# Kernel tuning notes

Hardware: AMD Instinct MI355X
Metric: run time of the kernel (lower is better)

The kernel has to match this reference:

```python
import jax, jax.numpy as jnp
import numpy as np

B, T, C = 2, 2048, 2048
H, HKV, D = 16, 4, 128
R = 64  # rope_dim = head_dim * rotary_pct


def setup_inputs() -> dict:
    key = jax.random.key(0)
    ks = jax.random.split(key, 8)
    s = 0.02
    return {
        "x": jax.random.normal(ks[0], (B, T, C), jnp.float32),
        "cos": jnp.cos(jax.random.normal(ks[1], (T, R), jnp.float32)),
        "sin": jnp.sin(jax.random.normal(ks[2], (T, R), jnp.float32)),
        "Wq": jax.random.normal(ks[3], (C, C), jnp.float32) * s,
        "Wk": jax.random.normal(ks[4], (C, HKV * D), jnp.float32) * s,
        "Wv": jax.random.normal(ks[5], (C, HKV * D), jnp.float32) * s,
        "Wo": jax.random.normal(ks[6], (C, C), jnp.float32) * s,
        "gate": jax.random.normal(ks[7], (H,), jnp.float32) * 0.1 - 3.0,
    }


def _rotate_half(t):
    t1, t2 = t[..., : t.shape[-1] // 2], t[..., t.shape[-1] // 2:]
    return jnp.concatenate([-t2, t1], axis=-1)


def reference(x, cos, sin, Wq, Wk, Wv, Wo, gate):
    # projections -> (B, heads, T, D)
    q = (x @ Wq).reshape(B, T, H, D).transpose(0, 2, 1, 3)
    k = (x @ Wk).reshape(B, T, HKV, D).transpose(0, 2, 1, 3)
    v = (x @ Wv).reshape(B, T, HKV, D).transpose(0, 2, 1, 3)

    # partial RoPE on first R dims; cos/sin (T,R) broadcast over (B,h,T,R)
    q_r = q[..., :R] * cos + _rotate_half(q[..., :R]) * sin
    k_r = k[..., :R] * cos + _rotate_half(k[..., :R]) * sin
    q = jnp.concatenate([q_r, q[..., R:]], axis=-1)
    k = jnp.concatenate([k_r, k[..., R:]], axis=-1)

    # GQA: repeat_interleave kv heads to match H
    rep = H // HKV
    k = jnp.repeat(k, rep, axis=1)
    v = jnp.repeat(v, rep, axis=1)

    scale = D ** -0.5
    att = jnp.einsum("bhtd,bhsd->bhts", q, k) * scale  # (B,H,T,T)
    causal = jnp.tril(jnp.ones((T, T), bool))
    att = jnp.where(causal, att, -jnp.inf)
    att = jax.nn.softmax(att, axis=-1)

    # post-softmax learned per-head threshold gate
    thr = jax.nn.sigmoid(gate)[None, :, None, None]
    att = att * (att >= thr).astype(att.dtype)

    y = jnp.einsum("bhts,bhsd->bhtd", att, v)
    y = y.transpose(0, 2, 1, 3).reshape(B, T, C)
    return y @ Wo
```

## Files before the change

### kernel.cpp

```cpp
#include <hip/hip_runtime.h>
#include <stdint.h>

#define Bdim 2
#define Tdim 2048
#define Cdim 2048
#define Hdim 16
#define HKVdim 4
#define KVdim 512
#define KT 32

typedef __attribute__((ext_vector_type(8))) short bf16x8;
typedef __attribute__((ext_vector_type(4))) float f32x4;

#define GLOAD16(gp, lp) __builtin_amdgcn_global_load_lds( \
    (const __attribute__((address_space(1))) void*)(gp),  \
    (__attribute__((address_space(3))) void*)(lp), 16, 0, 0)
#define WAITV(N) asm volatile("s_waitcnt vmcnt(" #N ")" ::: "memory")
#define WAITL0() asm volatile("s_waitcnt lgkmcnt(0)" ::: "memory")

__device__ __forceinline__ unsigned short f2bf(float f) {
  union { float f; unsigned u; } a; a.f = f;
  unsigned u = a.u + 0x7FFFu + ((a.u >> 16) & 1u);
  return (unsigned short)(u >> 16);
}
__device__ __forceinline__ float bf2f(unsigned short h) {
  union { float f; unsigned u; } a; a.u = ((unsigned)h) << 16;
  return a.f;
}

__global__ void split_x_kernel(const float* __restrict__ x, unsigned short* __restrict__ hi,
                               unsigned short* __restrict__ lo, int n) {
  int i = blockIdx.x * blockDim.x + threadIdx.x;
  int stride = gridDim.x * blockDim.x;
  for (; i < n; i += stride) {
    float f = x[i];
    unsigned short hb = f2bf(f);
    hi[i] = hb;
    lo[i] = f2bf(f - bf2f(hb));
  }
}

__global__ void transpose_split_kernel(const float* __restrict__ in, unsigned short* __restrict__ hi,
                                       unsigned short* __restrict__ lo, int K, int N) {
  __shared__ float tile[32][33];
  int k0 = blockIdx.x * 32, n0 = blockIdx.y * 32;
  int tx = threadIdx.x, ty = threadIdx.y;
#pragma unroll
  for (int i = 0; i < 32; i += 8)
    tile[ty + i][tx] = in[(size_t)(k0 + ty + i) * N + n0 + tx];
  __syncthreads();
#pragma unroll
  for (int i = 0; i < 32; i += 8) {
    float f = tile[tx][ty + i];
    size_t o = (size_t)(n0 + ty + i) * K + k0 + tx;
    unsigned short hb = f2bf(f);
    hi[o] = hb;
    if (lo) lo[o] = f2bf(f - bf2f(hb));
  }
}

__global__ __launch_bounds__(512, 4) void qkv8_kernel(
    const unsigned short* __restrict__ xhi, const unsigned short* __restrict__ xlo,
    const unsigned short* __restrict__ WqThi, const unsigned short* __restrict__ WqTlo,
    const unsigned short* __restrict__ WkThi, const unsigned short* __restrict__ WkTlo,
    const unsigned short* __restrict__ WvThi,
    const float* __restrict__ cs, const float* __restrict__ sn,
    unsigned short* __restrict__ qhi, unsigned short* __restrict__ qlo,
    unsigned short* __restrict__ khi, unsigned short* __restrict__ klo,
    unsigned short* __restrict__ vun)
{
  __shared__ char sL[3][24576];
  int tid = threadIdx.x, wid = tid >> 6, lane = tid & 63;
  int bid = blockIdx.x;
  int mode, bm, bn;
  if (bid < 256)      { mode = 0; bm = bid >> 3; bn = bid & 7; }
  else if (bid < 320) { int i = bid - 256; mode = 1; bm = i >> 1; bn = i & 1; }
  else                { int i = bid - 320; mode = 2; bm = i >> 1; bn = i & 1; }
  const unsigned short *Bhp, *Blp = WqTlo;
  if (mode == 0)      { Bhp = WqThi; Blp = WqTlo; }
  else if (mode == 1) { Bhp = WkThi; Blp = WkTlo; }
  else                { Bhp = WvThi; }
  int nk = (mode == 2) ? 64 : 192;

  const char* xh = (const char*)xhi;
  const char* xl = (const char*)xlo;
  const char* Bh = (const char*)Bhp;
  const char* Bl = (const char*)Blp;
  size_t arow0 = (size_t)bm * 128;
  size_t brow0 = (size_t)bn * 256;

  int wrow = (wid >> 2) & 1, wcol = wid & 3;
  int ln15 = lane & 15, j16 = (lane >> 4) * 16;

  f32x4 acc[4][4];
#pragma unroll
  for (int rf = 0; rf < 4; ++rf)
#pragma unroll
    for (int cf = 0; cf < 4; ++cf)
      acc[rf][cf] = f32x4{0.f, 0.f, 0.f, 0.f};

  auto stage = [&](int buf, int kt) {
    int reg = kt >> 6;
    int kk2 = (kt & 63) * 64;
    const char* As = (reg == 1) ? xl : xh;
    const char* Bs = (reg == 2) ? Bl : Bh;
    {
      int o = tid * 16; int row = o >> 6; int c = (o & 63) ^ ((row & 3) << 4);
      GLOAD16(As + (arow0 + row) * 4096 + kk2 + c, &sL[buf][o]);
    }
#pragma unroll
    for (int i = 0; i < 2; ++i) {
      int o = (i * 512 + tid) * 16; int row = o >> 6; int c = (o & 63) ^ ((row & 3) << 4);
      GLOAD16(Bs + (brow0 + row) * 4096 + kk2 + c, &sL[buf][8192 + o]);
    }
  };

  stage(0, 0); stage(1, 1); stage(2, 2);
  WAITV(6);
  __builtin_amdgcn_s_barrier();

  int cb = 0;
  for (int kt = 0; kt < nk; ++kt) {
    bf16x8 a[4], b[4];
    const char* base = sL[cb];
#pragma unroll
    for (int rf = 0; rf < 4; ++rf) {
      int r = wrow * 64 + rf * 16 + ln15;
      a[rf] = *(const bf16x8*)(base + r * 64 + (j16 ^ ((r & 3) << 4)));
    }
#pragma unroll
    for (int cf = 0; cf < 4; ++cf) {
      int r = wcol * 64 + cf * 16 + ln15;
      b[cf] = *(const bf16x8*)(base + 8192 + r * 64 + (j16 ^ ((r & 3) << 4)));
    }
    WAITL0();
    __builtin_amdgcn_sched_barrier(0);
    __builtin_amdgcn_s_barrier();
    if (kt + 3 < nk)      { stage(cb, kt + 3); WAITV(6); }
    else if (kt + 2 < nk) { WAITV(3); }
    else                  { WAITV(0); }
    __builtin_amdgcn_s_setprio(1);
#pragma unroll
    for (int rf = 0; rf < 4; ++rf)
#pragma unroll
      for (int cf = 0; cf < 4; ++cf)
        acc[rf][cf] = __builtin_amdgcn_mfma_f32_16x16x32_bf16(a[rf], b[cf], acc[rf][cf], 0, 0, 0);
    __builtin_amdgcn_s_setprio(0);
    __builtin_amdgcn_s_barrier();
    cb = (cb == 2) ? 0 : cb + 1;
  }

  if (mode <= 1) {
    int nh = (mode == 0) ? Hdim : HKVdim;
    unsigned short* oph = (mode == 0) ? qhi : khi;
    unsigned short* opl = (mode == 0) ? qlo : klo;
#pragma unroll
    for (int rf = 0; rf < 4; ++rf)
#pragma unroll
      for (int rr = 0; rr < 4; ++rr) {
        int rowl = wrow * 64 + rf * 16 + (lane >> 4) * 4 + rr;
        int grow = bm * 128 + rowl;
        int t = grow & (Tdim - 1), bb = grow >> 11;
#pragma unroll
        for (int cf = 0; cf < 4; ++cf) {
          int ncol = wcol * 64 + cf * 16 + ln15;
          int h = bn * 2 + (ncol >> 7);
          int d = ncol & 127;
          float o;
          if ((wcol & 1) == 0) {
            float c = cs[t * 64 + d], s = sn[t * 64 + d];
            o = (cf < 2) ? (acc[rf][cf][rr] * c - acc[rf][cf + 2][rr] * s)
                         : (acc[rf][cf][rr] * c + acc[rf][cf - 2][rr] * s);
          } else o = acc[rf][cf][rr];
          size_t ob = (((size_t)(bb * nh + h)) * Tdim + t) * 128 + d;
          unsigned short hb = f2bf(o);
          oph[ob] = hb;
          opl[ob] = f2bf(o - bf2f(hb));
        }
      }
  } else {
#pragma unroll
    for (int rf = 0; rf < 4; ++rf)
#pragma unroll
      for (int rr = 0; rr < 4; ++rr) {
        int rowl = wrow * 64 + rf * 16 + (lane >> 4) * 4 + rr;
        int grow = bm * 128 + rowl;
        int t = grow & (Tdim - 1), bb = grow >> 11;
#pragma unroll
        for (int cf = 0; cf < 4; ++cf) {
          int ncol = wcol * 64 + cf * 16 + ln15;
          int g = bn * 2 + (ncol >> 7);
          int d = ncol & 127;
          vun[(((size_t)(bb * HKVdim + g)) * Tdim + t) * 128 + d] = f2bf(acc[rf][cf][rr]);
        }
      }
  }
}

__global__ __launch_bounds__(512, 4) void wo8_kernel(
    const unsigned short* __restrict__ A, const unsigned short* __restrict__ Bt,
    float* __restrict__ C)
{
  __shared__ char sL[3][24576];
  int tid = threadIdx.x, wid = tid >> 6, lane = tid & 63;
  int bm = blockIdx.x >> 3, bn = blockIdx.x & 7;
  const char* As = (const char*)A;
  const char* Bs = (const char*)Bt;
  size_t arow0 = (size_t)bm * 128;
  size_t brow0 = (size_t)bn * 256;
  int wrow = (wid >> 2) & 1, wcol = wid & 3;
  int ln15 = lane & 15, j16 = (lane >> 4) * 16;
  const int nk = 64;

  f32x4 acc[4][4];
#pragma unroll
  for (int rf = 0; rf < 4; ++rf)
#pragma unroll
    for (int cf = 0; cf < 4; ++cf)
      acc[rf][cf] = f32x4{0.f, 0.f, 0.f, 0.f};

  auto stage = [&](int buf, int kt) {
    int kk2 = kt * 64;
    {
      int o = tid * 16; int row = o >> 6; int c = (o & 63) ^ ((row & 3) << 4);
      GLOAD16(As + (arow0 + row) * 4096 + kk2 + c, &sL[buf][o]);
    }
#pragma unroll
    for (int i = 0; i < 2; ++i) {
      int o = (i * 512 + tid) * 16; int row = o >> 6; int c = (o & 63) ^ ((row & 3) << 4);
      GLOAD16(Bs + (brow0 + row) * 4096 + kk2 + c, &sL[buf][8192 + o]);
    }
  };

  stage(0, 0); stage(1, 1); stage(2, 2);
  WAITV(6);
  __builtin_amdgcn_s_barrier();

  int cb = 0;
  for (int kt = 0; kt < nk; ++kt) {
    bf16x8 a[4], b[4];
    const char* base = sL[cb];
#pragma unroll
    for (int rf = 0; rf < 4; ++rf) {
      int r = wrow * 64 + rf * 16 + ln15;
      a[rf] = *(const bf16x8*)(base + r * 64 + (j16 ^ ((r & 3) << 4)));
    }
#pragma unroll
    for (int cf = 0; cf < 4; ++cf) {
      int r = wcol * 64 + cf * 16 + ln15;
      b[cf] = *(const bf16x8*)(base + 8192 + r * 64 + (j16 ^ ((r & 3) << 4)));
    }
    WAITL0();
    __builtin_amdgcn_sched_barrier(0);
    __builtin_amdgcn_s_barrier();
    if (kt + 3 < nk)      { stage(cb, kt + 3); WAITV(6); }
    else if (kt + 2 < nk) { WAITV(3); }
    else                  { WAITV(0); }
    __builtin_amdgcn_s_setprio(1);
#pragma unroll
    for (int rf = 0; rf < 4; ++rf)
#pragma unroll
      for (int cf = 0; cf < 4; ++cf)
        acc[rf][cf] = __builtin_amdgcn_mfma_f32_16x16x32_bf16(a[rf], b[cf], acc[rf][cf], 0, 0, 0);
    __builtin_amdgcn_s_setprio(0);
    __builtin_amdgcn_s_barrier();
    cb = (cb == 2) ? 0 : cb + 1;
  }

#pragma unroll
  for (int rf = 0; rf < 4; ++rf)
#pragma unroll
    for (int rr = 0; rr < 4; ++rr) {
      int grow = bm * 128 + wrow * 64 + rf * 16 + (lane >> 4) * 4 + rr;
#pragma unroll
      for (int cf = 0; cf < 4; ++cf) {
        int gcol = bn * 256 + wcol * 64 + cf * 16 + ln15;
        C[(size_t)grow * Cdim + gcol] = acc[rf][cf][rr];
      }
    }
}

__global__ void transpose_v_bf16_kernel(const unsigned short* __restrict__ vsrc,
                                        unsigned short* __restrict__ vt) {
  __shared__ unsigned short tile[32][33];
  int bg = blockIdx.x;
  int t0 = blockIdx.y * 32, d0 = blockIdx.z * 32;
  int tx = threadIdx.x, ty = threadIdx.y;
#pragma unroll
  for (int i = 0; i < 32; i += 8)
    tile[ty + i][tx] = vsrc[((size_t)bg * Tdim + t0 + ty + i) * 128 + d0 + tx];
  __syncthreads();
#pragma unroll
  for (int i = 0; i < 32; i += 8)
    vt[((size_t)(bg * 128 + d0 + ty + i)) * Tdim + t0 + tx] = tile[tx][ty + i];
}

__global__ __launch_bounds__(512, 4) void attn_kernel(
    const unsigned short* __restrict__ qhi, const unsigned short* __restrict__ qlo,
    const unsigned short* __restrict__ khi, const unsigned short* __restrict__ klo,
    const unsigned short* __restrict__ vt, const float* __restrict__ gate,
    unsigned short* __restrict__ y)
{
  __shared__ alignas(16) unsigned short sKh[2][KT * 128];
  __shared__ alignas(16) unsigned short sKl[2][KT * 128];
  __shared__ alignas(16) unsigned short sV[2][128 * KT];
  __shared__ alignas(16) unsigned short sP[8][16 * 40];
  __shared__ float sBM[8][64];

  int qb = (gridDim.x - 1) - blockIdx.x;
  int bh = blockIdx.y;
  int b = bh >> 4, h = bh & 15;
  int g = h >> 2;
  int t0 = qb * 128;
  int tid = threadIdx.x, wid = tid >> 6, lane = tid & 63;
  int ln15 = lane & 15, j16 = (lane >> 4) * 16, ro4 = (lane >> 4) * 4;
  const float cs2 = 0.08838834764831845f * 1.4426950408889634f;
  const float M2  = 8.0f * 1.4426950408889634f;

  const unsigned short* kh_base = khi + (((size_t)b * HKVdim + g) * Tdim) * 128;
  const unsigned short* kl_base = klo + (((size_t)b * HKVdim + g) * Tdim) * 128;
  const unsigned short* v_base  = vt  + (((size_t)b * HKVdim + g) * 128) * (size_t)Tdim;

  bf16x8 aqh[4], aql[4];
  {
    size_t qoff = ((((size_t)b * Hdim + h) * Tdim) + t0 + wid * 16 + ln15) * 128 + (lane >> 4) * 8;
#pragma unroll
    for (int kf = 0; kf < 4; ++kf) {
      aqh[kf] = *(const bf16x8*)(qhi + qoff + kf * 32);
      aql[kf] = *(const bf16x8*)(qlo + qoff + kf * 32);
    }
  }
  float thr = 1.f / (1.f + expf(-gate[h]));

  int nkb = (qb + 1) * 4;
  int tq_lo = t0 + wid * 16;

  auto stageK = [&](int buf, int kb) {
    int o = wid * 1024 + lane * 16;
    int row = o >> 8;
    int col = (o & 255) ^ ((row & 7) << 4);
    size_t goff = ((size_t)(kb * KT + row)) * 256 + col;
    GLOAD16((const char*)kh_base + goff, (char*)sKh[buf] + wid * 1024);
    GLOAD16((const char*)kl_base + goff, (char*)sKl[buf] + wid * 1024);
  };
  auto stageV = [&](int buf, int kb) {
    int o = wid * 1024 + lane * 16;
    int row = o >> 6;
    int col = (o & 63) ^ (((row ^ (row >> 2)) & 3) << 4);
    size_t goff = (size_t)row * (Tdim * 2) + (size_t)kb * 64 + col;
    GLOAD16((const char*)v_base + goff, (char*)sV[buf] + wid * 1024);
  };
  auto qk = [&](int buf, f32x4* s) {
    __builtin_amdgcn_s_setprio(1);
#pragma unroll
    for (int nf = 0; nf < 2; ++nf) {
      f32x4 a = {0.f, 0.f, 0.f, 0.f};
      int krow = nf * 16 + ln15;
      int sw = (krow & 7) << 4;
#pragma unroll
      for (int kf = 0; kf < 4; ++kf) {
        int boff = (kf * 64 + j16) ^ sw;
        bf16x8 bh_ = *(const bf16x8*)((const char*)sKh[buf] + krow * 256 + boff);
        bf16x8 bl_ = *(const bf16x8*)((const char*)sKl[buf] + krow * 256 + boff);
        a = __builtin_amdgcn_mfma_f32_16x16x32_bf16(aqh[kf], bh_, a, 0, 0, 0);
        a = __builtin_amdgcn_mfma_f32_16x16x32_bf16(aql[kf], bh_, a, 0, 0, 0);
        a = __builtin_amdgcn_mfma_f32_16x16x32_bf16(aqh[kf], bl_, a, 0, 0, 0);
      }
      s[nf] = a;
    }
    __builtin_amdgcn_s_setprio(0);
  };

  float lloc[4];
#pragma unroll
  for (int r = 0; r < 4; ++r) lloc[r] = 0.f;

  stageK(0, 0);
  __syncthreads();
  for (int kb = 0; kb < nkb; ++kb) {
    int buf = kb & 1;
    if (kb + 1 < nkb) stageK(buf ^ 1, kb + 1);
    if (kb * KT <= tq_lo + 15) {
      f32x4 s[2];
      qk(buf, s);
      float wmax = -1e30f;
      bool full = (kb * KT + KT - 1) <= tq_lo;
      if (full) {
#pragma unroll
        for (int nf = 0; nf < 2; ++nf)
#pragma unroll
          for (int r = 0; r < 4; ++r) {
            float v = s[nf][r] * cs2;
            wmax = fmaxf(wmax, v);
            lloc[r] += __builtin_exp2f(v - M2);
          }
      } else {
#pragma unroll
        for (int nf = 0; nf < 2; ++nf) {
          int tk = kb * KT + nf * 16 + ln15;
#pragma unroll
          for (int r = 0; r < 4; ++r) {
            int tq = tq_lo + ro4 + r;
            float v = (tk <= tq) ? s[nf][r] * cs2 : -1e30f;
            wmax = fmaxf(wmax, v);
            lloc[r] += __builtin_exp2f(v - M2);
          }
        }
      }
#pragma unroll
      for (int off = 1; off < 64; off <<= 1)
        wmax = fmaxf(wmax, __shfl_xor(wmax, off));
      if (lane == 0) sBM[wid][kb] = wmax;
    }
    __syncthreads();
  }

  float lrow[4], lgate2[4];
#pragma unroll
  for (int r = 0; r < 4; ++r) {
    float l = lloc[r];
#pragma unroll
    for (int off = 1; off < 16; off <<= 1) l += __shfl_xor(l, off);
    lrow[r] = l;
    lgate2[r] = __log2f(thr * l) + M2;
  }
  float lgmin = fminf(fminf(lgate2[0], lgate2[1]), fminf(lgate2[2], lgate2[3]));
  lgmin = fminf(lgmin, __shfl_xor(lgmin, 16));
  lgmin = fminf(lgmin, __shfl_xor(lgmin, 32));

  f32x4 yacc[8];
#pragma unroll
  for (int n = 0; n < 8; ++n) yacc[n] = f32x4{0.f, 0.f, 0.f, 0.f};

  stageK(0, 0);
  stageV(0, 0);
  __syncthreads();
  for (int kb = 0; kb < nkb; ++kb) {
    int buf = kb & 1;
    if (kb + 1 < nkb) { stageK(buf ^ 1, kb + 1); stageV(buf ^ 1, kb + 1); }
    if (kb * KT <= tq_lo + 15 && sBM[wid][kb] >= lgmin) {
      f32x4 s[2];
      qk(buf, s);
      bool anyk = false;
      float pv[2][4];
      bool full = (kb * KT + KT - 1) <= tq_lo;
#pragma unroll
      for (int nf = 0; nf < 2; ++nf) {
        int tk = kb * KT + nf * 16 + ln15;
#pragma unroll
        for (int r = 0; r < 4; ++r) {
          int tq = tq_lo + ro4 + r;
          float v = s[nf][r] * cs2;
          bool keep = (full || tk <= tq) && (v >= lgate2[r]);
          float p = 0.f;
          if (keep) { p = __builtin_exp2f(v - M2); anyk = true; }
          pv[nf][r] = p;
        }
      }
      if (__any(anyk)) {
#pragma unroll
        for (int nf = 0; nf < 2; ++nf)
#pragma unroll
          for (int r = 0; r < 4; ++r)
            sP[wid][(ro4 + r) * 40 + nf * 16 + ln15] = f2bf(pv[nf][r]);
        __builtin_amdgcn_s_setprio(1);
        bf16x8 pa = *(const bf16x8*)&sP[wid][ln15 * 40 + (lane >> 4) * 8];
#pragma unroll
        for (int nf2 = 0; nf2 < 8; ++nf2) {
          int vrow = nf2 * 16 + ln15;
          int vboff = j16 ^ (((vrow ^ (vrow >> 2)) & 3) << 4);
          bf16x8 vb = *(const bf16x8*)((const char*)sV[buf] + vrow * 64 + vboff);
          yacc[nf2] = __builtin_amdgcn_mfma_f32_16x16x32_bf16(pa, vb, yacc[nf2], 0, 0, 0);
        }
        __builtin_amdgcn_s_setprio(0);
      }
    }
    __syncthreads();
  }

#pragma unroll
  for (int r = 0; r < 4; ++r) {
    int tq = t0 + wid * 16 + ro4 + r;
    float invl = 1.f / lrow[r];
    size_t base = ((size_t)(b * Tdim + tq)) * Cdim + h * 128;
#pragma unroll
    for (int nf2 = 0; nf2 < 8; ++nf2)
      y[base + nf2 * 16 + ln15] = f2bf(yacc[nf2][r] * invl);
  }
}

extern "C" void kernel_launch(void* const* d_in, const int* in_sizes, int n_in,
                              void* d_out, int out_size, void* d_ws, size_t ws_size,
                              hipStream_t stream)
{
  (void)in_sizes; (void)n_in; (void)out_size; (void)ws_size;
  const float* x    = (const float*)d_in[0];
  const float* cosT = (const float*)d_in[1];
  const float* sinT = (const float*)d_in[2];
  const float* Wq   = (const float*)d_in[3];
  const float* Wk   = (const float*)d_in[4];
  const float* Wv   = (const float*)d_in[5];
  const float* Wo   = (const float*)d_in[6];
  const float* gate = (const float*)d_in[7];
  float* out = (float*)d_out;

  char* ws = (char*)d_ws;
  size_t off = 0;
  auto alloc = [&](size_t bytes) -> char* {
    char* p = ws + off; off += (bytes + 255) & ~(size_t)255; return p;
  };
  const size_t NX = (size_t)Bdim * Tdim * Cdim;
  const size_t NK = (size_t)Bdim * Tdim * KVdim;

  unsigned short* xhi   = (unsigned short*)alloc(NX * 2);
  unsigned short* xlo   = (unsigned short*)alloc(NX * 2);
  unsigned short* WqThi = (unsigned short*)alloc((size_t)Cdim * Cdim * 2);
  unsigned short* WqTlo = (unsigned short*)alloc((size_t)Cdim * Cdim * 2);
  unsigned short* WkThi = (unsigned short*)alloc((size_t)Cdim * KVdim * 2);
  unsigned short* WkTlo = (unsigned short*)alloc((size_t)Cdim * KVdim * 2);
  unsigned short* WvThi = (unsigned short*)alloc((size_t)Cdim * KVdim * 2);
  unsigned short* WoThi = (unsigned short*)alloc((size_t)Cdim * Cdim * 2);
  unsigned short* qhi   = (unsigned short*)alloc(NX * 2);
  unsigned short* qlo   = (unsigned short*)alloc(NX * 2);
  unsigned short* khi   = (unsigned short*)alloc(NK * 2);
  unsigned short* klo   = (unsigned short*)alloc(NK * 2);
  unsigned short* vun   = (unsigned short*)alloc(NK * 2);
  unsigned short* vtr   = (unsigned short*)alloc(NK * 2);
  unsigned short* yb    = (unsigned short*)alloc(NX * 2);

  dim3 tb(32, 8);
  split_x_kernel<<<2048, 256, 0, stream>>>(x, xhi, xlo, (int)NX);
  transpose_split_kernel<<<dim3(64, 64), tb, 0, stream>>>(Wq, WqThi, WqTlo, Cdim, Cdim);
  transpose_split_kernel<<<dim3(64, 16), tb, 0, stream>>>(Wk, WkThi, WkTlo, Cdim, KVdim);
  transpose_split_kernel<<<dim3(64, 16), tb, 0, stream>>>(Wv, WvThi, nullptr, Cdim, KVdim);
  transpose_split_kernel<<<dim3(64, 64), tb, 0, stream>>>(Wo, WoThi, nullptr, Cdim, Cdim);

  qkv8_kernel<<<384, 512, 0, stream>>>(
      xhi, xlo, WqThi, WqTlo, WkThi, WkTlo, WvThi,
      cosT, sinT, qhi, qlo, khi, klo, vun);
  transpose_v_bf16_kernel<<<dim3(8, 64, 4), tb, 0, stream>>>(vun, vtr);

  attn_kernel<<<dim3(16, 32), 512, 0, stream>>>(qhi, qlo, khi, klo, vtr, gate, yb);

  wo8_kernel<<<256, 512, 0, stream>>>(yb, WoThi, out);
}
```

Baseline: 427.4 us.

## Enlarge GEMM tiles to 256x256 with 4-stage split A/B ping-pong pipeline

Both the QKV and Wo GEMM kernels move from 128x256 to 256x256 output tiles per block, with each wave computing 128x64. Staging goes from a 3-buffer to a 4-buffer ring, and the A and B global-to-LDS loads are split so they interleave with two half-MFMA phases. The LDS swizzle pattern also changes. The aim is more operand reuse per LDS load and better overlap of loads with compute, at the cost of halving the grid (192 and 128 blocks on a 256-CU part), which leaves CUs idle and raises register and LDS pressure.

```diff
diff --git a/kernel.cpp b/kernel.cpp
--- a/kernel.cpp
+++ b/kernel.cpp
@@ -17,6 +17,7 @@
     (__attribute__((address_space(3))) void*)(lp), 16, 0, 0)
 #define WAITV(N) asm volatile("s_waitcnt vmcnt(" #N ")" ::: "memory")
 #define WAITL0() asm volatile("s_waitcnt lgkmcnt(0)" ::: "memory")
+#define SWZ(r) ((((r) >> 1) & 3) << 4)
 
 __device__ __forceinline__ unsigned short f2bf(float f) {
   union { float f; unsigned u; } a; a.f = f;
@@ -59,7 +60,8 @@
   }
 }
 
-__global__ __launch_bounds__(512, 4) void qkv8_kernel(
+
+__global__ __launch_bounds__(512, 2) void qkv8p_kernel(
     const unsigned short* __restrict__ xhi, const unsigned short* __restrict__ xlo,
     const unsigned short* __restrict__ WqThi, const unsigned short* __restrict__ WqTlo,
     const unsigned short* __restrict__ WkThi, const unsigned short* __restrict__ WkTlo,
@@ -69,13 +71,13 @@
     unsigned short* __restrict__ khi, unsigned short* __restrict__ klo,
     unsigned short* __restrict__ vun)
 {
-  __shared__ char sL[3][24576];
+  __shared__ char sL[4][32768];
   int tid = threadIdx.x, wid = tid >> 6, lane = tid & 63;
   int bid = blockIdx.x;
   int mode, bm, bn;
-  if (bid < 256)      { mode = 0; bm = bid >> 3; bn = bid & 7; }
-  else if (bid < 320) { int i = bid - 256; mode = 1; bm = i >> 1; bn = i & 1; }
-  else                { int i = bid - 320; mode = 2; bm = i >> 1; bn = i & 1; }
+  if (bid < 128)      { mode = 0; bm = bid >> 3; bn = bid & 7; }
+  else if (bid < 160) { int i = bid - 128; mode = 1; bm = i >> 1; bn = i & 1; }
+  else                { int i = bid - 160; mode = 2; bm = i >> 1; bn = i & 1; }
   const unsigned short *Bhp, *Blp = WqTlo;
   if (mode == 0)      { Bhp = WqThi; Blp = WqTlo; }
   else if (mode == 1) { Bhp = WkThi; Blp = WkTlo; }
@@ -86,68 +88,99 @@
   const char* xl = (const char*)xlo;
   const char* Bh = (const char*)Bhp;
   const char* Bl = (const char*)Blp;
-  size_t arow0 = (size_t)bm * 128;
+  size_t arow0 = (size_t)bm * 256;
   size_t brow0 = (size_t)bn * 256;
 
-  int wrow = (wid >> 2) & 1, wcol = wid & 3;
-  int ln15 = lane & 15, j16 = (lane >> 4) * 16;
-
-  f32x4 acc[4][4];
-#pragma unroll
-  for (int rf = 0; rf < 4; ++rf)
+  int wrow = wid >> 2, wcol = wid & 3;
+  int ln15 = lane & 15, cbk = (lane >> 4) * 16;
+
+  f32x4 acc[8][4];
+#pragma unroll
+  for (int rf = 0; rf < 8; ++rf)
 #pragma unroll
     for (int cf = 0; cf < 4; ++cf)
       acc[rf][cf] = f32x4{0.f, 0.f, 0.f, 0.f};
 
-  auto stage = [&](int buf, int kt) {
+  auto stageA = [&](int buf, int kt) {
     int reg = kt >> 6;
-    int kk2 = (kt & 63) * 64;
     const char* As = (reg == 1) ? xl : xh;
+    size_t kb = (size_t)(kt & 63) * 64;
+#pragma unroll
+    for (int i = 0; i < 2; ++i) {
+      int o = i * 8192 + tid * 16;
+      int row = o >> 6;
+      int c = (o & 63) ^ SWZ(row);
+      GLOAD16(As + (arow0 + row) * 4096 + kb + c, &sL[buf][o]);
+    }
+  };
+  auto stageB = [&](int buf, int kt) {
+    int reg = kt >> 6;
     const char* Bs = (reg == 2) ? Bl : Bh;
-    {
-      int o = tid * 16; int row = o >> 6; int c = (o & 63) ^ ((row & 3) << 4);
-      GLOAD16(As + (arow0 + row) * 4096 + kk2 + c, &sL[buf][o]);
-    }
+    size_t kb = (size_t)(kt & 63) * 64;
 #pragma unroll
     for (int i = 0; i < 2; ++i) {
-      int o = (i * 512 + tid) * 16; int row = o >> 6; int c = (o & 63) ^ ((row & 3) << 4);
-      GLOAD16(Bs + (brow0 + row) * 4096 + kk2 + c, &sL[buf][8192 + o]);
-    }
-  };
-
-  stage(0, 0); stage(1, 1); stage(2, 2);
-  WAITV(6);
+      int o = i * 8192 + tid * 16;
+      int row = o >> 6;
+      int c = (o & 63) ^ SWZ(row);
+      GLOAD16(Bs + (brow0 + row) * 4096 + kb + c, &sL[buf][16384 + o]);
+    }
+  };
+
+  stageA(0, 0); stageB(0, 0);
+  stageA(1, 1); stageB(1, 1);
+  stageA(2, 2); stageB(2, 2);
+  WAITV(8);
   __builtin_amdgcn_s_barrier();
 
-  int cb = 0;
-  for (int kt = 0; kt < nk; ++kt) {
-    bf16x8 a[4], b[4];
-    const char* base = sL[cb];
+  for (int j = 0; j < nk; ++j) {
+    const char* base = sL[j & 3];
+    int sb = (j + 3) & 3;
+    bf16x8 a0[4], a1[4], b[4];
 #pragma unroll
     for (int rf = 0; rf < 4; ++rf) {
-      int r = wrow * 64 + rf * 16 + ln15;
-      a[rf] = *(const bf16x8*)(base + r * 64 + (j16 ^ ((r & 3) << 4)));
+      int r = wrow * 128 + rf * 16 + ln15;
+      a0[rf] = *(const bf16x8*)(base + r * 64 + (cbk ^ SWZ(r)));
     }
 #pragma unroll
     for (int cf = 0; cf < 4; ++cf) {
       int r = wcol * 64 + cf * 16 + ln15;
-      b[cf] = *(const bf16x8*)(base + 8192 + r * 64 + (j16 ^ ((r & 3) << 4)));
-    }
+      b[cf] = *(const bf16x8*)(base + 16384 + r * 64 + (cbk ^ SWZ(r)));
+    }
+    if (j + 3 < nk) stageA(sb, j + 3);
+    __builtin_amdgcn_s_barrier();
     WAITL0();
     __builtin_amdgcn_sched_barrier(0);
-    __builtin_amdgcn_s_barrier();
-    if (kt + 3 < nk)      { stage(cb, kt + 3); WAITV(6); }
-    else if (kt + 2 < nk) { WAITV(3); }
-    else                  { WAITV(0); }
     __builtin_amdgcn_s_setprio(1);
 #pragma unroll
     for (int rf = 0; rf < 4; ++rf)
 #pragma unroll
       for (int cf = 0; cf < 4; ++cf)
-        acc[rf][cf] = __builtin_amdgcn_mfma_f32_16x16x32_bf16(a[rf], b[cf], acc[rf][cf], 0, 0, 0);
+        acc[rf][cf] = __builtin_amdgcn_mfma_f32_16x16x32_bf16(a0[rf], b[cf], acc[rf][cf], 0, 0, 0);
     __builtin_amdgcn_s_setprio(0);
     __builtin_amdgcn_s_barrier();
-    cb = (cb == 2) ? 0 : cb + 1;
+#pragma unroll
+    for (int rf = 0; rf < 4; ++rf) {
+      int r = wrow * 128 + 64 + rf * 16 + ln15;
+      a1[rf] = *(const bf16x8*)(base + r * 64 + (cbk ^ SWZ(r)));
+    }
+    if (j + 3 < nk) stageB(sb, j + 3);
+    __builtin_amdgcn_s_barrier();
+    WAITL0();
+    __builtin_amdgcn_sched_barrier(0);
+    __builtin_amdgcn_s_setprio(1);
+#pragma unroll
+    for (int rf = 0; rf < 4; ++rf)
+#pragma unroll
+      for (int cf = 0; cf < 4; ++cf)
+        acc[rf + 4][cf] = __builtin_amdgcn_mfma_f32_16x16x32_bf16(a1[rf], b[cf], acc[rf + 4][cf], 0, 0, 0);
+    __builtin_amdgcn_s_setprio(0);
+    {
+      int rem = nk - j - 2;
+      if (rem >= 2)      { WAITV(8); }
+      else if (rem == 1) { WAITV(4); }
+      else if (rem == 0) { WAITV(0); }
+    }
+    __builtin_amdgcn_s_barrier();
   }
 
   if (mode <= 1) {
@@ -155,11 +188,10 @@
     unsigned short* oph = (mode == 0) ? qhi : khi;
     unsigned short* opl = (mode == 0) ? qlo : klo;
 #pragma unroll
-    for (int rf = 0; rf < 4; ++rf)
+    for (int rf = 0; rf < 8; ++rf)
 #pragma unroll
       for (int rr = 0; rr < 4; ++rr) {
-        int rowl = wrow * 64 + rf * 16 + (lane >> 4) * 4 + rr;
-        int grow = bm * 128 + rowl;
+        int grow = bm * 256 + wrow * 128 + rf * 16 + (lane >> 4) * 4 + rr;
         int t = grow & (Tdim - 1), bb = grow >> 11;
 #pragma unroll
         for (int cf = 0; cf < 4; ++cf) {
@@ -180,11 +212,10 @@
       }
   } else {
 #pragma unroll
-    for (int rf = 0; rf < 4; ++rf)
+    for (int rf = 0; rf < 8; ++rf)
 #pragma unroll
       for (int rr = 0; rr < 4; ++rr) {
-        int rowl = wrow * 64 + rf * 16 + (lane >> 4) * 4 + rr;
-        int grow = bm * 128 + rowl;
+        int grow = bm * 256 + wrow * 128 + rf * 16 + (lane >> 4) * 4 + rr;
         int t = grow & (Tdim - 1), bb = grow >> 11;
 #pragma unroll
         for (int cf = 0; cf < 4; ++cf) {
@@ -197,81 +228,111 @@
   }
 }
 
-__global__ __launch_bounds__(512, 4) void wo8_kernel(
+__global__ __launch_bounds__(512, 2) void wo8p_kernel(
     const unsigned short* __restrict__ A, const unsigned short* __restrict__ Bt,
     float* __restrict__ C)
 {
-  __shared__ char sL[3][24576];
+  __shared__ char sL[4][32768];
   int tid = threadIdx.x, wid = tid >> 6, lane = tid & 63;
   int bm = blockIdx.x >> 3, bn = blockIdx.x & 7;
   const char* As = (const char*)A;
   const char* Bs = (const char*)Bt;
-  size_t arow0 = (size_t)bm * 128;
+  size_t arow0 = (size_t)bm * 256;
   size_t brow0 = (size_t)bn * 256;
-  int wrow = (wid >> 2) & 1, wcol = wid & 3;
-  int ln15 = lane & 15, j16 = (lane >> 4) * 16;
+  int wrow = wid >> 2, wcol = wid & 3;
+  int ln15 = lane & 15, cbk = (lane >> 4) * 16;
   const int nk = 64;
 
-  f32x4 acc[4][4];
-#pragma unroll
-  for (int rf = 0; rf < 4; ++rf)
+  f32x4 acc[8][4];
+#pragma unroll
+  for (int rf = 0; rf < 8; ++rf)
 #pragma unroll
     for (int cf = 0; cf < 4; ++cf)
       acc[rf][cf] = f32x4{0.f, 0.f, 0.f, 0.f};
 
-  auto stage = [&](int buf, int kt) {
-    int kk2 = kt * 64;
-    {
-      int o = tid * 16; int row = o >> 6; int c = (o & 63) ^ ((row & 3) << 4);
-      GLOAD16(As + (arow0 + row) * 4096 + kk2 + c, &sL[buf][o]);
-    }
+  auto stageA = [&](int buf, int kt) {
+    size_t kb = (size_t)kt * 64;
 #pragma unroll
     for (int i = 0; i < 2; ++i) {
-      int o = (i * 512 + tid) * 16; int row = o >> 6; int c = (o & 63) ^ ((row & 3) << 4);
-      GLOAD16(Bs + (brow0 + row) * 4096 + kk2 + c, &sL[buf][8192 + o]);
-    }
-  };
-
-  stage(0, 0); stage(1, 1); stage(2, 2);
-  WAITV(6);
+      int o = i * 8192 + tid * 16;
+      int row = o >> 6;
+      int c = (o & 63) ^ SWZ(row);
+      GLOAD16(As + (arow0 + row) * 4096 + kb + c, &sL[buf][o]);
+    }
+  };
+  auto stageB = [&](int buf, int kt) {
+    size_t kb = (size_t)kt * 64;
+#pragma unroll
+    for (int i = 0; i < 2; ++i) {
+      int o = i * 8192 + tid * 16;
+      int row = o >> 6;
+      int c = (o & 63) ^ SWZ(row);
+      GLOAD16(Bs + (brow0 + row) * 4096 + kb + c, &sL[buf][16384 + o]);
+    }
+  };
+
+  stageA(0, 0); stageB(0, 0);
+  stageA(1, 1); stageB(1, 1);
+  stageA(2, 2); stageB(2, 2);
+  WAITV(8);
   __builtin_amdgcn_s_barrier();
 
-  int cb = 0;
-  for (int kt = 0; kt < nk; ++kt) {
-    bf16x8 a[4], b[4];
-    const char* base = sL[cb];
+  for (int j = 0; j < nk; ++j) {
+    const char* base = sL[j & 3];
+    int sb = (j + 3) & 3;
+    bf16x8 a0[4], a1[4], b[4];
 #pragma unroll
     for (int rf = 0; rf < 4; ++rf) {
-      int r = wrow * 64 + rf * 16 + ln15;
-      a[rf] = *(const bf16x8*)(base + r * 64 + (j16 ^ ((r & 3) << 4)));
+      int r = wrow * 128 + rf * 16 + ln15;
+      a0[rf] = *(const bf16x8*)(base + r * 64 + (cbk ^ SWZ(r)));
     }
 #pragma unroll
     for (int cf = 0; cf < 4; ++cf) {
       int r = wcol * 64 + cf * 16 + ln15;
-      b[cf] = *(const bf16x8*)(base + 8192 + r * 64 + (j16 ^ ((r & 3) << 4)));
-    }
+      b[cf] = *(const bf16x8*)(base + 16384 + r * 64 + (cbk ^ SWZ(r)));
+    }
+    if (j + 3 < nk) stageA(sb, j + 3);
+    __builtin_amdgcn_s_barrier();
     WAITL0();
     __builtin_amdgcn_sched_barrier(0);
-    __builtin_amdgcn_s_barrier();
-    if (kt + 3 < nk)      { stage(cb, kt + 3); WAITV(6); }
-    else if (kt + 2 < nk) { WAITV(3); }
-    else                  { WAITV(0); }
     __builtin_amdgcn_s_setprio(1);
 #pragma unroll
     for (int rf = 0; rf < 4; ++rf)
 #pragma unroll
       for (int cf = 0; cf < 4; ++cf)
-        acc[rf][cf] = __builtin_amdgcn_mfma_f32_16x16x32_bf16(a[rf], b[cf], acc[rf][cf], 0, 0, 0);
+        acc[rf][cf] = __builtin_amdgcn_mfma_f32_16x16x32_bf16(a0[rf], b[cf], acc[rf][cf], 0, 0, 0);
     __builtin_amdgcn_s_setprio(0);
     __builtin_amdgcn_s_barrier();
-    cb = (cb == 2) ? 0 : cb + 1;
-  }
-
-#pragma unroll
-  for (int rf = 0; rf < 4; ++rf)
+#pragma unroll
+    for (int rf = 0; rf < 4; ++rf) {
+      int r = wrow * 128 + 64 + rf * 16 + ln15;
+      a1[rf] = *(const bf16x8*)(base + r * 64 + (cbk ^ SWZ(r)));
+    }
+    if (j + 3 < nk) stageB(sb, j + 3);
+    __builtin_amdgcn_s_barrier();
+    WAITL0();
+    __builtin_amdgcn_sched_barrier(0);
+    __builtin_amdgcn_s_setprio(1);
+#pragma unroll
+    for (int rf = 0; rf < 4; ++rf)
+#pragma unroll
+      for (int cf = 0; cf < 4; ++cf)
+        acc[rf + 4][cf] = __builtin_amdgcn_mfma_f32_16x16x32_bf16(a1[rf], b[cf], acc[rf + 4][cf], 0, 0, 0);
+    __builtin_amdgcn_s_setprio(0);
+    {
+      int rem = nk - j - 2;
+      if (rem >= 2)      { WAITV(8); }
+      else if (rem == 1) { WAITV(4); }
+      else if (rem == 0) { WAITV(0); }
+    }
+    __builtin_amdgcn_s_barrier();
+  }
+
+#pragma unroll
+  for (int rf = 0; rf < 8; ++rf)
 #pragma unroll
     for (int rr = 0; rr < 4; ++rr) {
-      int grow = bm * 128 + wrow * 64 + rf * 16 + (lane >> 4) * 4 + rr;
+      int grow = bm * 256 + wrow * 128 + rf * 16 + (lane >> 4) * 4 + rr;
 #pragma unroll
       for (int cf = 0; cf < 4; ++cf) {
         int gcol = bn * 256 + wcol * 64 + cf * 16 + ln15;
@@ -535,12 +596,12 @@
   transpose_split_kernel<<<dim3(64, 16), tb, 0, stream>>>(Wv, WvThi, nullptr, Cdim, KVdim);
   transpose_split_kernel<<<dim3(64, 64), tb, 0, stream>>>(Wo, WoThi, nullptr, Cdim, Cdim);
 
-  qkv8_kernel<<<384, 512, 0, stream>>>(
+  qkv8p_kernel<<<192, 512, 0, stream>>>(
       xhi, xlo, WqThi, WqTlo, WkThi, WkTlo, WvThi,
       cosT, sinT, qhi, qlo, khi, klo, vun);
   transpose_v_bf16_kernel<<<dim3(8, 64, 4), tb, 0, stream>>>(vun, vtr);
 
   attn_kernel<<<dim3(16, 32), 512, 0, stream>>>(qhi, qlo, khi, klo, vtr, gate, yb);
 
-  wo8_kernel<<<256, 512, 0, stream>>>(yb, WoThi, out);
-}
+  wo8p_kernel<<<128, 512, 0, stream>>>(yb, WoThi, out);
+}
```

Measured after the change: 450.1 us. 1.05x slower.
